# Performance work log

Measured on AMD Instinct MI355X. Metric: run time of the kernel, lower is better.

## Reference

```python
import jax, jax.numpy as jnp
import numpy as np
import math

DIM, NH, HD = 4096, 32, 128
B, S = 2, 2048
MAX_SEQ, INIT_SLICE = 4096, 2048  # init_slice = max_seq_len - max_prompt_size
NEG = -1e9


def setup_inputs() -> dict:
    key = jax.random.key(0)
    ks = jax.random.split(key, 6)
    x = jax.random.normal(ks[0], (B, S, DIM), dtype=jnp.float32)
    scale = 1.0 / math.sqrt(DIM)
    wq = jax.random.normal(ks[1], (DIM, DIM), dtype=jnp.float32) * scale
    wk = jax.random.normal(ks[2], (DIM, DIM), dtype=jnp.float32) * scale
    wv = jax.random.normal(ks[3], (DIM, DIM), dtype=jnp.float32) * scale
    wo = jax.random.normal(ks[4], (DIM, DIM), dtype=jnp.float32) * scale
    # RoPE frequencies, viewed as real pairs [S, HD//2, 2] = (cos, sin)
    inv_freq = 1.0 / (10000.0 ** (jnp.arange(0, HD, 2, dtype=jnp.float32) / HD))
    ang = jnp.arange(S, dtype=jnp.float32)[:, None] * inv_freq[None, :]  # [S, HD//2]
    freqs_cis_real = jnp.stack([jnp.cos(ang), jnp.sin(ang)], axis=-1)
    # causal additive mask [1,1,S,S]
    mask = jnp.where(jnp.triu(jnp.ones((S, S), dtype=bool), k=1), NEG, 0.0)[None, None].astype(jnp.float32)
    cache_k = jnp.zeros((B, MAX_SEQ, NH, HD), dtype=jnp.float32)
    cache_v = jnp.zeros((B, MAX_SEQ, NH, HD), dtype=jnp.float32)
    return {"x": x, "freqs_cis_real": freqs_cis_real, "mask": mask,
            "wq": wq, "wk": wk, "wv": wv, "wo": wo,
            "cache_k": cache_k, "cache_v": cache_v, "slice_size": 2048}


def _apply_rotary(xq, xk, freqs_cis_real):
    # xq, xk: [b, s, h, d]; pairs along last dim are (real, imag)
    b, s, h, d = xq.shape
    fr = freqs_cis_real[None, :, None, :, 0]  # [1, s, 1, d//2]
    fi = freqs_cis_real[None, :, None, :, 1]

    def rot(t):
        t = t.reshape(b, s, h, d // 2, 2)
        tr, ti = t[..., 0], t[..., 1]
        out = jnp.stack([tr * fr - ti * fi, tr * fi + ti * fr], axis=-1)
        return out.reshape(b, s, h, d)

    return rot(xq), rot(xk)


def reference(x, freqs_cis_real, mask, wq, wk, wv, wo, cache_k, cache_v, slice_size):
    bsz, seqlen, _ = x.shape
    xq = (x @ wq.T).reshape(bsz, seqlen, NH, HD)
    xk = (x @ wk.T).reshape(bsz, seqlen, NH, HD)
    xv = (x @ wv.T).reshape(bsz, seqlen, NH, HD)
    xq, xk = _apply_rotary(xq, xk, freqs_cis_real)
    # prompt-phase (seqlen > 1) cache update: cat(cache[:, :init_slice], new)
    cache_k_new = jnp.concatenate([cache_k[:bsz, :INIT_SLICE], xk], axis=1)
    cache_v_new = jnp.concatenate([cache_v[:bsz, :INIT_SLICE], xv], axis=1)
    keys = cache_k_new[:, -slice_size:]    # [b, k, h, d]
    values = cache_v_new[:, -slice_size:]
    scores = jnp.einsum('bqhd,bkhd->bhqk', xq, keys) / math.sqrt(HD)
    scores = scores + mask
    probs = jax.nn.softmax(scores.astype(jnp.float32), axis=-1).astype(xq.dtype)
    out = jnp.einsum('bhqk,bkhd->bqhd', probs, values).reshape(bsz, seqlen, -1)
    return out @ wo.T
```

## Files before the change

### kernel.cpp

```cpp
#include <hip/hip_runtime.h>
#include <hip/hip_bf16.h>
#include <stdint.h>

#define SEQ   2048
#define NHEAD 32
#define HDIM  128
#define DMODEL 4096
#define MTOT  4096
#define RSCALE 0.08838834764831845f

typedef __hip_bfloat16 bf16_t;
typedef __attribute__((ext_vector_type(8))) short short8v;
typedef __attribute__((ext_vector_type(4))) short short4v;
typedef __attribute__((ext_vector_type(4))) float f32x4;
typedef __attribute__((ext_vector_type(2))) float f32x2;

typedef __attribute__((address_space(3))) void lds_void;
typedef __attribute__((address_space(1))) void gbl_void;
#define TO_LDS(p) ((lds_void*)(uint32_t)(uintptr_t)(p))
#define TO_GBL(p) ((gbl_void*)(uintptr_t)(p))
#define ASYNC_CP16(g, l) __builtin_amdgcn_global_load_lds(TO_GBL(g), TO_LDS(l), 16, 0, 0)

__device__ __forceinline__ float bf2f(short u) {
  union { uint32_t i; float f; } x; x.i = ((uint32_t)(uint16_t)u) << 16; return x.f;
}

__global__ __launch_bounds__(256) void cast4_f32_to_bf16(const float* __restrict__ s0,
                                                         const float* __restrict__ s1,
                                                         const float* __restrict__ s2,
                                                         const float* __restrict__ s3,
                                                         bf16_t* __restrict__ out) {
  const int w = blockIdx.y;
  const float* in = (w == 0) ? s0 : ((w == 1) ? s1 : ((w == 2) ? s2 : s3));
  bf16_t* o = out + (size_t)w * 16777216u;
  size_t i = (size_t)blockIdx.x * 256 + threadIdx.x;
  const f32x4* p = (const f32x4*)in + i * 2;
  f32x4 a = p[0], b = p[1];
  __align__(16) bf16_t tmp[8];
#pragma unroll
  for (int j = 0; j < 4; ++j) tmp[j]     = __float2bfloat16(a[j]);
#pragma unroll
  for (int j = 0; j < 4; ++j) tmp[4 + j] = __float2bfloat16(b[j]);
  *(short8v*)(o + i * 8) = *(const short8v*)tmp;
}

#define VMW_(N) asm volatile("s_waitcnt vmcnt(" #N ")" ::: "memory")
#define VMW(N) VMW_(N)
#define SB0 __builtin_amdgcn_sched_barrier(0)

#define STAGE_A(mh_, X)                                                        \
  { const int tr_ = tid >> 3, c_ = tid & 7;                                    \
    _Pragma("unroll")                                                          \
    for (int i_ = 0; i_ < 2; ++i_) {                                           \
      const int row_ = (mh_) * 64 + i_ * 128 + tr_;                            \
      const int cg_ = c_ ^ (row_ & 7);                                         \
      ASYNC_CP16(gA0 + (size_t)row_ * 4096 + (size_t)(X) * 64 + cg_ * 8,       \
                 ldsc + (((X) & 1) << 16) + row_ * 128 + c_ * 16); } }

#define STAGE_B(nh_, X)                                                        \
  { const int tr_ = tid >> 3, c_ = tid & 7;                                    \
    _Pragma("unroll")                                                          \
    for (int i_ = 0; i_ < 2; ++i_) {                                           \
      const int row_ = i_ * 128 + (tr_ >> 5) * 64 + (nh_) * 32 + (tr_ & 31);   \
      const int cg_ = c_ ^ (row_ & 7);                                         \
      ASYNC_CP16(gB0 + (size_t)row_ * 4096 + (size_t)(X) * 64 + cg_ * 8,       \
                 ldsc + (((X) & 1) << 16) + 32768 + row_ * 128 + c_ * 16); } }

#define TILE4(T, DOSTG, VA, VB, VC)                                            \
  {                                                                            \
    const int sb = ((T) & 1) << 16;                                            \
    const int Xn = (T) + 1;                                                    \
    short8v a0[4][2], a1[4][2], b0[2][2], b1[2][2];                            \
                                                 \
    VMW(VA);                                                                   \
    __builtin_amdgcn_s_barrier();                                              \
    SB0;                                                                       \
    _Pragma("unroll") for (int m = 0; m < 4; ++m)                              \
      _Pragma("unroll") for (int kk = 0; kk < 2; ++kk)                         \
        a0[m][kk] = *(const short8v*)(ldsc + sb + aRow + m * 2048 + (kk ? cx1 : cx0)); \
    _Pragma("unroll") for (int n = 0; n < 2; ++n)                              \
      _Pragma("unroll") for (int kk = 0; kk < 2; ++kk)                         \
        b0[n][kk] = *(const short8v*)(ldsc + sb + bRow + n * 2048 + (kk ? cx1 : cx0)); \
    if (DOSTG) STAGE_A(0, Xn);                                                 \
    asm volatile("s_waitcnt lgkmcnt(0)" ::: "memory");                         \
    SB0;                                                                       \
    __builtin_amdgcn_s_setprio(1);                                             \
    _Pragma("unroll") for (int m = 0; m < 4; ++m)                              \
      _Pragma("unroll") for (int n = 0; n < 2; ++n)                            \
        _Pragma("unroll") for (int kk = 0; kk < 2; ++kk)                       \
          acc[m][n] = __builtin_amdgcn_mfma_f32_16x16x32_bf16(a0[m][kk], b0[n][kk], acc[m][n], 0, 0, 0); \
    __builtin_amdgcn_s_setprio(0);                                             \
                                                 \
    VMW(VB);                                                                   \
    __builtin_amdgcn_s_barrier();                                              \
    SB0;                                                                       \
    _Pragma("unroll") for (int n = 0; n < 2; ++n)                              \
      _Pragma("unroll") for (int kk = 0; kk < 2; ++kk)                         \
        b1[n][kk] = *(const short8v*)(ldsc + sb + bRow + 4096 + n * 2048 + (kk ? cx1 : cx0)); \
    if (DOSTG) STAGE_B(0, Xn);                                                 \
    asm volatile("s_waitcnt lgkmcnt(0)" ::: "memory");                         \
    SB0;                                                                       \
    __builtin_amdgcn_s_setprio(1);                                             \
    _Pragma("unroll") for (int m = 0; m < 4; ++m)                              \
      _Pragma("unroll") for (int n = 0; n < 2; ++n)                            \
        _Pragma("unroll") for (int kk = 0; kk < 2; ++kk)                       \
          acc[m][2 + n] = __builtin_amdgcn_mfma_f32_16x16x32_bf16(a0[m][kk], b1[n][kk], acc[m][2 + n], 0, 0, 0); \
    __builtin_amdgcn_s_setprio(0);                                             \
                                                 \
    VMW(VC);                                                                   \
    __builtin_amdgcn_s_barrier();                                              \
    SB0;                                                                       \
    _Pragma("unroll") for (int m = 0; m < 4; ++m)                              \
      _Pragma("unroll") for (int kk = 0; kk < 2; ++kk)                         \
        a1[m][kk] = *(const short8v*)(ldsc + sb + aRow + 8192 + m * 2048 + (kk ? cx1 : cx0)); \
    if (DOSTG) STAGE_B(1, Xn);                                                 \
    asm volatile("s_waitcnt lgkmcnt(0)" ::: "memory");                         \
    SB0;                                                                       \
    __builtin_amdgcn_s_setprio(1);                                             \
    _Pragma("unroll") for (int m = 0; m < 4; ++m)                              \
      _Pragma("unroll") for (int n = 0; n < 2; ++n)                            \
        _Pragma("unroll") for (int kk = 0; kk < 2; ++kk)                       \
          acc[4 + m][2 + n] = __builtin_amdgcn_mfma_f32_16x16x32_bf16(a1[m][kk], b1[n][kk], acc[4 + m][2 + n], 0, 0, 0); \
    __builtin_amdgcn_s_setprio(0);                                             \
                                     \
    if (DOSTG) STAGE_A(1, Xn);                                                 \
    __builtin_amdgcn_s_setprio(1);                                             \
    _Pragma("unroll") for (int m = 0; m < 4; ++m)                              \
      _Pragma("unroll") for (int n = 0; n < 2; ++n)                            \
        _Pragma("unroll") for (int kk = 0; kk < 2; ++kk)                       \
          acc[4 + m][n] = __builtin_amdgcn_mfma_f32_16x16x32_bf16(a1[m][kk], b0[n][kk], acc[4 + m][n], 0, 0, 0); \
    __builtin_amdgcn_s_setprio(0);                                             \
  }

template <int MODE>
__global__ __launch_bounds__(512, 2) void gemm_nt(const bf16_t* __restrict__ A,
                                                  const bf16_t* __restrict__ B0,
                                                  const bf16_t* __restrict__ B1,
                                                  const bf16_t* __restrict__ B2,
                                                  void* __restrict__ out0,
                                                  bf16_t* __restrict__ out1,
                                                  bf16_t* __restrict__ out2,
                                                  const float* __restrict__ freqs) {
  __shared__ __align__(16) char ldsbuf[131072];
  char* ldsc = ldsbuf;
  const int z = blockIdx.z;
  const bf16_t* __restrict__ Bm = (z == 0) ? B0 : (z == 1 ? B1 : B2);
  const int tid = threadIdx.x;
  const int wave = tid >> 6, lane = tid & 63;
  const int bid = blockIdx.x;
  const int xcd = bid & 7, idx = bid >> 3;
  const int bm = xcd * 2 + (idx >> 4);
  const int bn = idx & 15;
  const int wr = wave >> 2, wc = wave & 3;
  const int r = lane & 15, g = lane >> 4;

  f32x4 acc[8][4] = {};

  const bf16_t* gA0 = A  + (size_t)bm * 256 * 4096;
  const bf16_t* gB0 = Bm + (size_t)bn * 256 * 4096;

  const int swz = r & 7;
  const int cx0 = (g ^ swz) << 4;
  const int cx1 = ((4 + g) ^ swz) << 4;
  const int aRow = (wr * 128 + r) * 128;
  const int bRow = 32768 + (wc * 64 + r) * 128;

  STAGE_A(0, 0);
  STAGE_B(0, 0);
  STAGE_B(1, 0);
  STAGE_A(1, 0);

  for (int T = 0; T < 63; ++T) TILE4(T, 1, 4, 4, 4);
  TILE4(63, 0, 4, 2, 0);

  const int row0 = bm * 256 + wr * 128 + g * 4;
  const int col0 = bn * 256 + wc * 64;

  if (MODE == 0) {
    float* C = (float*)out0;
#pragma unroll
    for (int m = 0; m < 8; ++m)
#pragma unroll
      for (int n = 0; n < 4; ++n)
#pragma unroll
        for (int j = 0; j < 4; ++j)
          C[(size_t)(row0 + m * 16 + j) * 4096 + col0 + n * 16 + r] = acc[m][n][j];
  } else if (z == 2) {
    bf16_t* VT = out2;
#pragma unroll
    for (int m = 0; m < 8; ++m) {
      const int row = row0 + m * 16;
      const int b = row >> 11, s = row & 2047;
#pragma unroll
      for (int n = 0; n < 4; ++n) {
        const int col = col0 + n * 16 + r;
        const int h = col >> 7, d = col & 127;
        __align__(8) bf16_t tp[4];
#pragma unroll
        for (int j = 0; j < 4; ++j) tp[j] = __float2bfloat16(acc[m][n][j]);
        *(short4v*)&VT[((size_t)(b * 32 + h) * 128 + d) * 2048 + s] = *(const short4v*)tp;
      }
    }
  } else if (z == 0) {
    bf16_t* dst = (bf16_t*)out0;
#pragma unroll
    for (int m = 0; m < 8; ++m)
#pragma unroll
      for (int j = 0; j < 4; ++j) {
        const int row = row0 + m * 16 + j;
        const int b = row >> 11, s = row & 2047;
#pragma unroll
        for (int n = 0; n < 4; ++n) {
          const int col = col0 + n * 16 + r;
          const int h = col >> 7, d = col & 127;
          dst[((size_t)(b * 32 + h) * 2048 + s) * 128 + d] = __float2bfloat16(acc[m][n][j]);
        }
      }
  } else {
    bf16_t* dst = out1;
    const float sgn = (r & 1) ? 1.0f : -1.0f;
#pragma unroll
    for (int m = 0; m < 8; ++m)
#pragma unroll
      for (int j = 0; j < 4; ++j) {
        const int row = row0 + m * 16 + j;
        const int b = row >> 11, s = row & 2047;
#pragma unroll
        for (int n = 0; n < 4; ++n) {
          const int col = col0 + n * 16 + r;
          const int h = col >> 7, d = col & 127;
          const float self = acc[m][n][j];
          const float part = __shfl_xor(self, 1, 64);
          const float* fp = freqs + (size_t)s * 128 + (d >> 1) * 2;
          const float frv = fp[0];
          const float fiv = fp[1] * sgn;
          dst[((size_t)(b * 32 + h) * 2048 + s) * 128 + d] =
              __float2bfloat16(self * frv + part * fiv);
        }
      }
  }
}

__global__ __launch_bounds__(512) void attn_kernel(const bf16_t* __restrict__ qrot,
                                                   const bf16_t* __restrict__ krot,
                                                   const bf16_t* __restrict__ vt,
                                                   const float* __restrict__ freqs,
                                                   bf16_t* __restrict__ att,
                                                   const float* __restrict__ wo_src,
                                                   bf16_t* __restrict__ wo_dst) {
  __shared__ bf16_t Kls[2][64 * 128];
  __shared__ bf16_t Vls[2][128 * 64];
  __shared__ bf16_t Pls[8][16 * 64];

  if (blockIdx.x >= 1024) {
    const int cb = blockIdx.x - 1024;
    const int tid = threadIdx.x;
#pragma unroll
    for (int p = 0; p < 8; ++p) {
      size_t i = ((size_t)p * 512 + cb) * 512 + tid;
      const f32x4* pp = (const f32x4*)wo_src + i * 2;
      f32x4 a = pp[0], b = pp[1];
      __align__(16) bf16_t tmp[8];
#pragma unroll
      for (int j = 0; j < 4; ++j) tmp[j]     = __float2bfloat16(a[j]);
#pragma unroll
      for (int j = 0; j < 4; ++j) tmp[4 + j] = __float2bfloat16(b[j]);
      *(short8v*)(wo_dst + i * 8) = *(const short8v*)tmp;
    }
    return;
  }

  const int lid  = blockIdx.x;
  const int xcd  = lid & 7;
  const int kk_  = lid >> 3;
  const int bh   = xcd + 8 * ((kk_ >> 4) & 7);
  const int qidx = 15 - (kk_ & 15);
  const int warp = threadIdx.x >> 6;
  const int lane = threadIdx.x & 63;
  const int r = lane & 15, g = lane >> 4;

  const bf16_t* __restrict__ Q  = qrot + (size_t)bh * 2048 * 128;
  const bf16_t* __restrict__ Kp = krot + (size_t)bh * 2048 * 128;
  const bf16_t* __restrict__ Vt = vt   + (size_t)bh * 128 * 2048;
  char* __restrict__ Pb = (char*)&Pls[warp][0];

  const int qB = qidx * 128 + warp * 16;
  const int ntiles = 2 * qidx + 2;
  const int psw = (r & 7) << 4;

  short8v qf[4];
  {
    const int s = qB + r;
    const float* fbase = freqs + (size_t)s * 128;
#pragma unroll
    for (int kk = 0; kk < 4; ++kk) {
      short8v qraw = *(const short8v*)&Q[(size_t)s * 128 + kk * 32 + g * 8];
      __align__(16) bf16_t qt[8];
#pragma unroll
      for (int i = 0; i < 4; ++i) {
        const int p = kk * 16 + g * 4 + i;
        f32x2 cs = *(const f32x2*)(fbase + p * 2);
        const float a = bf2f(qraw[2 * i]), b = bf2f(qraw[2 * i + 1]);
        qt[2 * i]     = __float2bfloat16((a * cs[0] - b * cs[1]) * RSCALE);
        qt[2 * i + 1] = __float2bfloat16((a * cs[1] + b * cs[0]) * RSCALE);
      }
      qf[kk] = *(const short8v*)qt;
    }
  }

  float l = 0.f;
  f32x4 o[8];
#pragma unroll
  for (int n2 = 0; n2 < 8; ++n2) o[n2] = f32x4{0.f, 0.f, 0.f, 0.f};

  const int rA = lane >> 4, cA = lane & 15;
  const int rB = lane >> 3, cB = lane & 7;
  const int swz = (r & 7) << 4;

  auto STG = [&](int kb_, int buf) {
#pragma unroll
    for (int i = 0; i < 2; ++i) {
      const int krow = warp * 8 + i * 4 + rA;
      const int kcol = 8 * (cA ^ (krow & 7));
      ASYNC_CP16(Kp + (size_t)(kb_ + krow) * 128 + kcol,
                 (char*)&Kls[buf][0] + (size_t)(krow * 128 + cA * 8) * 2);
    }
#pragma unroll
    for (int i = 0; i < 2; ++i) {
      const int vrow = warp * 16 + i * 8 + rB;
      const int vcol = 8 * (cB ^ rB);
      ASYNC_CP16(Vt + (size_t)vrow * 2048 + kb_ + vcol,
                 (char*)&Vls[buf][0] + (size_t)(vrow * 64 + cB * 8) * 2);
    }
  };

  STG(0, 0);
  VMW(0);
  __builtin_amdgcn_s_barrier();
  int cur = 0;
  for (int t = 0; t < ntiles; ++t) {
    const int kb = t * 64;
    if (t + 1 < ntiles) STG(kb + 64, cur ^ 1);

    if (kb <= qB + 15) {
      const char* Kc = (const char*)&Kls[cur][0];
      const char* Vc = (const char*)&Vls[cur][0];
      f32x4 sacc[4];
#pragma unroll
      for (int n = 0; n < 4; ++n) sacc[n] = f32x4{0.f, 0.f, 0.f, 0.f};
#pragma unroll
      for (int n = 0; n < 4; ++n)
#pragma unroll
        for (int kk = 0; kk < 4; ++kk) {
          short8v kf = *(const short8v*)(Kc + (n * 16 + r) * 256 + ((kk * 64 + g * 16) ^ swz));
          sacc[n] = __builtin_amdgcn_mfma_f32_16x16x32_bf16(kf, qf[kk], sacc[n], 0, 0, 0);
        }

      float p[16];
#pragma unroll
      for (int n = 0; n < 4; ++n)
#pragma unroll
        for (int j = 0; j < 4; ++j)
          p[n * 4 + j] = __expf(sacc[n][j]);

      if (kb + 63 > qB) {
        const int qa = qB + r;
#pragma unroll
        for (int n = 0; n < 4; ++n)
#pragma unroll
          for (int j = 0; j < 4; ++j)
            if (kb + n * 16 + g * 4 + j > qa) p[n * 4 + j] = 0.f;
      }

      {
        float ts[8];
#pragma unroll
        for (int i = 0; i < 8; ++i) ts[i] = p[i] + p[i + 8];
#pragma unroll
        for (int i = 0; i < 4; ++i) ts[i] += ts[i + 4];
        float rs = (ts[0] + ts[1]) + (ts[2] + ts[3]);
        rs += __shfl_xor(rs, 16, 64);
        rs += __shfl_xor(rs, 32, 64);
        l += rs;
      }

#pragma unroll
      for (int n = 0; n < 4; ++n) {
        __align__(8) bf16_t tp[4];
#pragma unroll
        for (int j = 0; j < 4; ++j) tp[j] = __float2bfloat16(p[n * 4 + j]);
        *(short4v*)(Pb + r * 128 + ((n * 32 + g * 8) ^ psw)) = *(const short4v*)tp;
      }

#pragma unroll
      for (int kk2 = 0; kk2 < 2; ++kk2) {
        short8v pf = *(const short8v*)(Pb + r * 128 + ((kk2 * 64 + g * 16) ^ psw));
#pragma unroll
        for (int n2 = 0; n2 < 8; ++n2) {
          short8v vf = *(const short8v*)(Vc + (n2 * 16 + r) * 128 + ((kk2 * 64 + g * 16) ^ swz));
          o[n2] = __builtin_amdgcn_mfma_f32_16x16x32_bf16(pf, vf, o[n2], 0, 0, 0);
        }
      }
    }

    if (t + 1 < ntiles) {
      VMW(0);
      __builtin_amdgcn_s_barrier();
    }
    cur ^= 1;
  }

  float lq[4];
#pragma unroll
  for (int j = 0; j < 4; ++j) lq[j] = 1.0f / __shfl(l, g * 4 + j, 64);
  const int b = bh >> 5, h = bh & 31;
#pragma unroll
  for (int n2 = 0; n2 < 8; ++n2)
#pragma unroll
    for (int j = 0; j < 4; ++j)
      att[((size_t)(b * 2048 + qB + g * 4 + j)) * 4096 + h * 128 + n2 * 16 + r] =
          __float2bfloat16(o[n2][j] * lq[j]);
}

extern "C" void kernel_launch(void* const* d_in, const int* in_sizes, int n_in,
                              void* d_out, int out_size, void* d_ws, size_t ws_size,
                              hipStream_t stream) {
  (void)in_sizes; (void)n_in; (void)out_size; (void)ws_size;
  const float* x  = (const float*)d_in[0];
  const float* fr = (const float*)d_in[1];
  const float* wq = (const float*)d_in[3];
  const float* wk = (const float*)d_in[4];
  const float* wv = (const float*)d_in[5];
  const float* wo = (const float*)d_in[6];

  char* ws = (char*)d_ws;
  const size_t MB32 = 33554432;
  bf16_t* xb   = (bf16_t*)(ws + 0 * MB32);
  bf16_t* wqb  = (bf16_t*)(ws + 1 * MB32);
  bf16_t* wkb  = (bf16_t*)(ws + 2 * MB32);
  bf16_t* wvb  = (bf16_t*)(ws + 3 * MB32);
  bf16_t* qrot = (bf16_t*)(ws + 4 * MB32);
  bf16_t* krot = (bf16_t*)(ws + 5 * MB32);
  bf16_t* vtp  = (bf16_t*)(ws + 6 * MB32);

  cast4_f32_to_bf16<<<dim3(8192, 4), 256, 0, stream>>>(x, wq, wk, wv, xb);

  gemm_nt<1><<<dim3(256, 1, 3), 512, 0, stream>>>(xb, wqb, wkb, wvb,
                                                  (void*)qrot, krot, vtp, fr);

  bf16_t* wob  = wqb;
  bf16_t* attb = xb;

  attn_kernel<<<1536, 512, 0, stream>>>(qrot, krot, vtp, fr, attb, wo, wob);

  gemm_nt<0><<<dim3(256, 1, 1), 512, 0, stream>>>(attb, wob, wob, wob,
                                                  d_out, nullptr, nullptr, nullptr);
}
```

Before: 629.2 us.

## Load GEMM A operand directly from global into registers, stage only B in LDS

The projection GEMM kernel no longer stages the A tile through LDS. Each wave now loads its A fragments straight from global memory into registers, double-buffered across k-steps, while only the B tile is staged asynchronously into a halved LDS buffer. The wave layout also changes from 2x4 to 4x2 with 64x128 per-wave tiles, and the per-tile barriers drop from three to one. This cuts LDS traffic, LDS footprint and synchronisation, at the cost of uncoalesced global loads for A, more register pressure, and redundant A reads by the two waves that share each row block.

```diff
diff --git a/kernel.cpp b/kernel.cpp
--- a/kernel.cpp
+++ b/kernel.cpp
@@ -24,6 +24,10 @@
 __device__ __forceinline__ float bf2f(short u) {
   union { uint32_t i; float f; } x; x.i = ((uint32_t)(uint16_t)u) << 16; return x.f;
 }
+
+#define VMW_(N) asm volatile("s_waitcnt vmcnt(" #N ")" ::: "memory")
+#define VMW(N) VMW_(N)
+#define SB0 __builtin_amdgcn_sched_barrier(0)
 
 __global__ __launch_bounds__(256) void cast4_f32_to_bf16(const float* __restrict__ s0,
                                                          const float* __restrict__ s1,
@@ -44,92 +48,44 @@
   *(short8v*)(o + i * 8) = *(const short8v*)tmp;
 }
 
-#define VMW_(N) asm volatile("s_waitcnt vmcnt(" #N ")" ::: "memory")
-#define VMW(N) VMW_(N)
-#define SB0 __builtin_amdgcn_sched_barrier(0)
-
-#define STAGE_A(mh_, X)                                                        \
+#define STAGE_BT(slot_, X)                                                     \
   { const int tr_ = tid >> 3, c_ = tid & 7;                                    \
     _Pragma("unroll")                                                          \
-    for (int i_ = 0; i_ < 2; ++i_) {                                           \
-      const int row_ = (mh_) * 64 + i_ * 128 + tr_;                            \
-      const int cg_ = c_ ^ (row_ & 7);                                         \
-      ASYNC_CP16(gA0 + (size_t)row_ * 4096 + (size_t)(X) * 64 + cg_ * 8,       \
-                 ldsc + (((X) & 1) << 16) + row_ * 128 + c_ * 16); } }
-
-#define STAGE_B(nh_, X)                                                        \
-  { const int tr_ = tid >> 3, c_ = tid & 7;                                    \
-    _Pragma("unroll")                                                          \
-    for (int i_ = 0; i_ < 2; ++i_) {                                           \
-      const int row_ = i_ * 128 + (tr_ >> 5) * 64 + (nh_) * 32 + (tr_ & 31);   \
+    for (int i_ = 0; i_ < 4; ++i_) {                                           \
+      const int row_ = i_ * 64 + tr_;                                          \
       const int cg_ = c_ ^ (row_ & 7);                                         \
       ASYNC_CP16(gB0 + (size_t)row_ * 4096 + (size_t)(X) * 64 + cg_ * 8,       \
-                 ldsc + (((X) & 1) << 16) + 32768 + row_ * 128 + c_ * 16); } }
-
-#define TILE4(T, DOSTG, VA, VB, VC)                                            \
+                 ldsc + (slot_) * 32768 + row_ * 128 + c_ * 16); } }
+
+#define LDA(AR, X)                                                             \
+  _Pragma("unroll") for (int m_ = 0; m_ < 4; ++m_)                             \
+    _Pragma("unroll") for (int kk_ = 0; kk_ < 2; ++kk_)                        \
+      AR[m_][kk_] = *(const short8v*)(gA0 + (size_t)m_ * 65536 +               \
+                                      (size_t)(X) * 64 + kk_ * 32 + g * 8);
+
+#define GTILE(TT, AC, AN, DOSTG)                                               \
   {                                                                            \
-    const int sb = ((T) & 1) << 16;                                            \
-    const int Xn = (T) + 1;                                                    \
-    short8v a0[4][2], a1[4][2], b0[2][2], b1[2][2];                            \
-                                                 \
-    VMW(VA);                                                                   \
-    __builtin_amdgcn_s_barrier();                                              \
-    SB0;                                                                       \
-    _Pragma("unroll") for (int m = 0; m < 4; ++m)                              \
-      _Pragma("unroll") for (int kk = 0; kk < 2; ++kk)                         \
-        a0[m][kk] = *(const short8v*)(ldsc + sb + aRow + m * 2048 + (kk ? cx1 : cx0)); \
-    _Pragma("unroll") for (int n = 0; n < 2; ++n)                              \
-      _Pragma("unroll") for (int kk = 0; kk < 2; ++kk)                         \
-        b0[n][kk] = *(const short8v*)(ldsc + sb + bRow + n * 2048 + (kk ? cx1 : cx0)); \
-    if (DOSTG) STAGE_A(0, Xn);                                                 \
-    asm volatile("s_waitcnt lgkmcnt(0)" ::: "memory");                         \
-    SB0;                                                                       \
+    const int slot_c = (TT) & 1;                                               \
+    if (DOSTG) {                                                               \
+      STAGE_BT(slot_c ^ 1, (TT) + 1);                                          \
+      LDA(AN, (TT) + 1);                                                       \
+    }                                                                          \
     __builtin_amdgcn_s_setprio(1);                                             \
-    _Pragma("unroll") for (int m = 0; m < 4; ++m)                              \
-      _Pragma("unroll") for (int n = 0; n < 2; ++n)                            \
-        _Pragma("unroll") for (int kk = 0; kk < 2; ++kk)                       \
-          acc[m][n] = __builtin_amdgcn_mfma_f32_16x16x32_bf16(a0[m][kk], b0[n][kk], acc[m][n], 0, 0, 0); \
+    _Pragma("unroll") for (int n = 0; n < 8; ++n) {                            \
+      const char* bp = ldsc + slot_c * 32768 + bRow + n * 2048;                \
+      short8v b0 = *(const short8v*)(bp + cx0);                                \
+      short8v b1 = *(const short8v*)(bp + cx1);                                \
+      _Pragma("unroll") for (int m = 0; m < 4; ++m) {                          \
+        acc[m][n] = __builtin_amdgcn_mfma_f32_16x16x32_bf16(AC[m][0], b0, acc[m][n], 0, 0, 0); \
+        acc[m][n] = __builtin_amdgcn_mfma_f32_16x16x32_bf16(AC[m][1], b1, acc[m][n], 0, 0, 0); \
+      }                                                                        \
+    }                                                                          \
     __builtin_amdgcn_s_setprio(0);                                             \
-                                                 \
-    VMW(VB);                                                                   \
-    __builtin_amdgcn_s_barrier();                                              \
-    SB0;                                                                       \
-    _Pragma("unroll") for (int n = 0; n < 2; ++n)                              \
-      _Pragma("unroll") for (int kk = 0; kk < 2; ++kk)                         \
-        b1[n][kk] = *(const short8v*)(ldsc + sb + bRow + 4096 + n * 2048 + (kk ? cx1 : cx0)); \
-    if (DOSTG) STAGE_B(0, Xn);                                                 \
-    asm volatile("s_waitcnt lgkmcnt(0)" ::: "memory");                         \
-    SB0;                                                                       \
-    __builtin_amdgcn_s_setprio(1);                                             \
-    _Pragma("unroll") for (int m = 0; m < 4; ++m)                              \
-      _Pragma("unroll") for (int n = 0; n < 2; ++n)                            \
-        _Pragma("unroll") for (int kk = 0; kk < 2; ++kk)                       \
-          acc[m][2 + n] = __builtin_amdgcn_mfma_f32_16x16x32_bf16(a0[m][kk], b1[n][kk], acc[m][2 + n], 0, 0, 0); \
-    __builtin_amdgcn_s_setprio(0);                                             \
-                                                 \
-    VMW(VC);                                                                   \
-    __builtin_amdgcn_s_barrier();                                              \
-    SB0;                                                                       \
-    _Pragma("unroll") for (int m = 0; m < 4; ++m)                              \
-      _Pragma("unroll") for (int kk = 0; kk < 2; ++kk)                         \
-        a1[m][kk] = *(const short8v*)(ldsc + sb + aRow + 8192 + m * 2048 + (kk ? cx1 : cx0)); \
-    if (DOSTG) STAGE_B(1, Xn);                                                 \
-    asm volatile("s_waitcnt lgkmcnt(0)" ::: "memory");                         \
-    SB0;                                                                       \
-    __builtin_amdgcn_s_setprio(1);                                             \
-    _Pragma("unroll") for (int m = 0; m < 4; ++m)                              \
-      _Pragma("unroll") for (int n = 0; n < 2; ++n)                            \
-        _Pragma("unroll") for (int kk = 0; kk < 2; ++kk)                       \
-          acc[4 + m][2 + n] = __builtin_amdgcn_mfma_f32_16x16x32_bf16(a1[m][kk], b1[n][kk], acc[4 + m][2 + n], 0, 0, 0); \
-    __builtin_amdgcn_s_setprio(0);                                             \
-                                     \
-    if (DOSTG) STAGE_A(1, Xn);                                                 \
-    __builtin_amdgcn_s_setprio(1);                                             \
-    _Pragma("unroll") for (int m = 0; m < 4; ++m)                              \
-      _Pragma("unroll") for (int n = 0; n < 2; ++n)                            \
-        _Pragma("unroll") for (int kk = 0; kk < 2; ++kk)                       \
-          acc[4 + m][n] = __builtin_amdgcn_mfma_f32_16x16x32_bf16(a1[m][kk], b0[n][kk], acc[4 + m][n], 0, 0, 0); \
-    __builtin_amdgcn_s_setprio(0);                                             \
+    if (DOSTG) {                                                               \
+      VMW(8);                                                                  \
+      __builtin_amdgcn_s_barrier();                                            \
+      SB0;                                                                     \
+    }                                                                          \
   }
 
 template <int MODE>
@@ -141,7 +97,7 @@
                                                   bf16_t* __restrict__ out1,
                                                   bf16_t* __restrict__ out2,
                                                   const float* __restrict__ freqs) {
-  __shared__ __align__(16) char ldsbuf[131072];
+  __shared__ __align__(16) char ldsbuf[65536];
   char* ldsc = ldsbuf;
   const int z = blockIdx.z;
   const bf16_t* __restrict__ Bm = (z == 0) ? B0 : (z == 1 ? B1 : B2);
@@ -151,48 +107,54 @@
   const int xcd = bid & 7, idx = bid >> 3;
   const int bm = xcd * 2 + (idx >> 4);
   const int bn = idx & 15;
-  const int wr = wave >> 2, wc = wave & 3;
+  const int wr = wave >> 1, wc = wave & 1;
   const int r = lane & 15, g = lane >> 4;
 
-  f32x4 acc[8][4] = {};
-
-  const bf16_t* gA0 = A  + (size_t)bm * 256 * 4096;
+  f32x4 acc[4][8] = {};
+
+  const bf16_t* gA0 = A + ((size_t)(bm * 256 + wr * 64 + r)) * 4096;
   const bf16_t* gB0 = Bm + (size_t)bn * 256 * 4096;
 
   const int swz = r & 7;
   const int cx0 = (g ^ swz) << 4;
   const int cx1 = ((4 + g) ^ swz) << 4;
-  const int aRow = (wr * 128 + r) * 128;
-  const int bRow = 32768 + (wc * 64 + r) * 128;
-
-  STAGE_A(0, 0);
-  STAGE_B(0, 0);
-  STAGE_B(1, 0);
-  STAGE_A(1, 0);
-
-  for (int T = 0; T < 63; ++T) TILE4(T, 1, 4, 4, 4);
-  TILE4(63, 0, 4, 2, 0);
-
-  const int row0 = bm * 256 + wr * 128 + g * 4;
-  const int col0 = bn * 256 + wc * 64;
+  const int bRow = (wc * 128 + r) * 128;
+
+  short8v aA[4][2], aB[4][2];
+
+  STAGE_BT(0, 0);
+  LDA(aA, 0);
+  VMW(8);
+  __builtin_amdgcn_s_barrier();
+  SB0;
+
+  for (int T = 0; T < 62; T += 2) {
+    GTILE(T, aA, aB, 1);
+    GTILE(T + 1, aB, aA, 1);
+  }
+  GTILE(62, aA, aB, 1);
+  GTILE(63, aB, aA, 0);
+
+  const int row0 = bm * 256 + wr * 64 + g * 4;
+  const int col0 = bn * 256 + wc * 128;
 
   if (MODE == 0) {
     float* C = (float*)out0;
 #pragma unroll
-    for (int m = 0; m < 8; ++m)
-#pragma unroll
-      for (int n = 0; n < 4; ++n)
+    for (int m = 0; m < 4; ++m)
+#pragma unroll
+      for (int n = 0; n < 8; ++n)
 #pragma unroll
         for (int j = 0; j < 4; ++j)
           C[(size_t)(row0 + m * 16 + j) * 4096 + col0 + n * 16 + r] = acc[m][n][j];
   } else if (z == 2) {
     bf16_t* VT = out2;
 #pragma unroll
-    for (int m = 0; m < 8; ++m) {
+    for (int m = 0; m < 4; ++m) {
       const int row = row0 + m * 16;
       const int b = row >> 11, s = row & 2047;
 #pragma unroll
-      for (int n = 0; n < 4; ++n) {
+      for (int n = 0; n < 8; ++n) {
         const int col = col0 + n * 16 + r;
         const int h = col >> 7, d = col & 127;
         __align__(8) bf16_t tp[4];
@@ -204,13 +166,13 @@
   } else if (z == 0) {
     bf16_t* dst = (bf16_t*)out0;
 #pragma unroll
-    for (int m = 0; m < 8; ++m)
+    for (int m = 0; m < 4; ++m)
 #pragma unroll
       for (int j = 0; j < 4; ++j) {
         const int row = row0 + m * 16 + j;
         const int b = row >> 11, s = row & 2047;
 #pragma unroll
-        for (int n = 0; n < 4; ++n) {
+        for (int n = 0; n < 8; ++n) {
           const int col = col0 + n * 16 + r;
           const int h = col >> 7, d = col & 127;
           dst[((size_t)(b * 32 + h) * 2048 + s) * 128 + d] = __float2bfloat16(acc[m][n][j]);
@@ -220,13 +182,13 @@
     bf16_t* dst = out1;
     const float sgn = (r & 1) ? 1.0f : -1.0f;
 #pragma unroll
-    for (int m = 0; m < 8; ++m)
+    for (int m = 0; m < 4; ++m)
 #pragma unroll
       for (int j = 0; j < 4; ++j) {
         const int row = row0 + m * 16 + j;
         const int b = row >> 11, s = row & 2047;
 #pragma unroll
-        for (int n = 0; n < 4; ++n) {
+        for (int n = 0; n < 8; ++n) {
           const int col = col0 + n * 16 + r;
           const int h = col >> 7, d = col & 127;
           const float self = acc[m][n][j];
```

New measurement: 866.8 us. 37.8% more time.

## Restructure GEMM main loop into deeper prefetch pipeline with split-phase barriers

Applied to the files above, without the earlier changes.

Rewrites the bf16 NT GEMM inner loop so global-to-LDS async copies for tile T+2 are issued while tile T is computed, with tile T+1's B half staged early. Each of the four 64x... quadrant MFMA phases is bracketed by barriers and LDS reads are overlapped with outstanding loads via partial lgkmcnt waits. The intent is to hide global memory latency better and keep MFMA units busier, at the cost of more barriers per k-tile and tighter vmcnt bookkeeping that could serialize if miscounted.

```diff
diff --git a/kernel.cpp b/kernel.cpp
--- a/kernel.cpp
+++ b/kernel.cpp
@@ -24,6 +24,12 @@
 __device__ __forceinline__ float bf2f(short u) {
   union { uint32_t i; float f; } x; x.i = ((uint32_t)(uint16_t)u) << 16; return x.f;
 }
+
+#define VMW_(N) asm volatile("s_waitcnt vmcnt(" #N ")" ::: "memory")
+#define VMW(N) VMW_(N)
+#define SB0 __builtin_amdgcn_sched_barrier(0)
+#define LGKM0 asm volatile("s_waitcnt lgkmcnt(0)" ::: "memory")
+#define LGKM8 asm volatile("s_waitcnt lgkmcnt(8)" ::: "memory")
 
 __global__ __launch_bounds__(256) void cast4_f32_to_bf16(const float* __restrict__ s0,
                                                          const float* __restrict__ s1,
@@ -44,10 +50,6 @@
   *(short8v*)(o + i * 8) = *(const short8v*)tmp;
 }
 
-#define VMW_(N) asm volatile("s_waitcnt vmcnt(" #N ")" ::: "memory")
-#define VMW(N) VMW_(N)
-#define SB0 __builtin_amdgcn_sched_barrier(0)
-
 #define STAGE_A(mh_, X)                                                        \
   { const int tr_ = tid >> 3, c_ = tid & 7;                                    \
     _Pragma("unroll")                                                          \
@@ -66,70 +68,56 @@
       ASYNC_CP16(gB0 + (size_t)row_ * 4096 + (size_t)(X) * 64 + cg_ * 8,       \
                  ldsc + (((X) & 1) << 16) + 32768 + row_ * 128 + c_ * 16); } }
 
-#define TILE4(T, DOSTG, VA, VB, VC)                                            \
+#define RD_A(AR, SL, MH)                                                       \
+  _Pragma("unroll") for (int m_ = 0; m_ < 4; ++m_) {                           \
+    AR[m_][0] = *(const short8v*)(ldsc + (SL) + aRow + (MH) * 8192 + m_ * 2048 + cx0); \
+    AR[m_][1] = *(const short8v*)(ldsc + (SL) + aRow + (MH) * 8192 + m_ * 2048 + cx1); }
+
+#define RD_B(BR, SL, NH)                                                       \
+  _Pragma("unroll") for (int n_ = 0; n_ < 2; ++n_) {                           \
+    BR[n_][0] = *(const short8v*)(ldsc + (SL) + bRow + (NH) * 4096 + n_ * 2048 + cx0); \
+    BR[n_][1] = *(const short8v*)(ldsc + (SL) + bRow + (NH) * 4096 + n_ * 2048 + cx1); }
+
+#define MFMA16(AR, BR, MH, NH)                                                 \
+  __builtin_amdgcn_s_setprio(1);                                               \
+  _Pragma("unroll") for (int m_ = 0; m_ < 4; ++m_)                             \
+    _Pragma("unroll") for (int n_ = 0; n_ < 2; ++n_) {                         \
+      acc[(MH)*4+m_][(NH)*2+n_] = __builtin_amdgcn_mfma_f32_16x16x32_bf16(     \
+          AR[m_][0], BR[n_][0], acc[(MH)*4+m_][(NH)*2+n_], 0, 0, 0);           \
+      acc[(MH)*4+m_][(NH)*2+n_] = __builtin_amdgcn_mfma_f32_16x16x32_bf16(     \
+          AR[m_][1], BR[n_][1], acc[(MH)*4+m_][(NH)*2+n_], 0, 0, 0); }         \
+  __builtin_amdgcn_s_setprio(0);
+
+#define BAR __builtin_amdgcn_s_barrier()
+
+#define KTILE(T, SB1_, SA0_, SB0_, SA1_, VMC)                                  \
   {                                                                            \
-    const int sb = ((T) & 1) << 16;                                            \
-    const int Xn = (T) + 1;                                                    \
-    short8v a0[4][2], a1[4][2], b0[2][2], b1[2][2];                            \
-                                                 \
-    VMW(VA);                                                                   \
-    __builtin_amdgcn_s_barrier();                                              \
-    SB0;                                                                       \
-    _Pragma("unroll") for (int m = 0; m < 4; ++m)                              \
-      _Pragma("unroll") for (int kk = 0; kk < 2; ++kk)                         \
-        a0[m][kk] = *(const short8v*)(ldsc + sb + aRow + m * 2048 + (kk ? cx1 : cx0)); \
-    _Pragma("unroll") for (int n = 0; n < 2; ++n)                              \
-      _Pragma("unroll") for (int kk = 0; kk < 2; ++kk)                         \
-        b0[n][kk] = *(const short8v*)(ldsc + sb + bRow + n * 2048 + (kk ? cx1 : cx0)); \
-    if (DOSTG) STAGE_A(0, Xn);                                                 \
-    asm volatile("s_waitcnt lgkmcnt(0)" ::: "memory");                         \
-    SB0;                                                                       \
-    __builtin_amdgcn_s_setprio(1);                                             \
-    _Pragma("unroll") for (int m = 0; m < 4; ++m)                              \
-      _Pragma("unroll") for (int n = 0; n < 2; ++n)                            \
-        _Pragma("unroll") for (int kk = 0; kk < 2; ++kk)                       \
-          acc[m][n] = __builtin_amdgcn_mfma_f32_16x16x32_bf16(a0[m][kk], b0[n][kk], acc[m][n], 0, 0, 0); \
-    __builtin_amdgcn_s_setprio(0);                                             \
-                                                 \
-    VMW(VB);                                                                   \
-    __builtin_amdgcn_s_barrier();                                              \
-    SB0;                                                                       \
-    _Pragma("unroll") for (int n = 0; n < 2; ++n)                              \
-      _Pragma("unroll") for (int kk = 0; kk < 2; ++kk)                         \
-        b1[n][kk] = *(const short8v*)(ldsc + sb + bRow + 4096 + n * 2048 + (kk ? cx1 : cx0)); \
-    if (DOSTG) STAGE_B(0, Xn);                                                 \
-    asm volatile("s_waitcnt lgkmcnt(0)" ::: "memory");                         \
-    SB0;                                                                       \
-    __builtin_amdgcn_s_setprio(1);                                             \
-    _Pragma("unroll") for (int m = 0; m < 4; ++m)                              \
-      _Pragma("unroll") for (int n = 0; n < 2; ++n)                            \
-        _Pragma("unroll") for (int kk = 0; kk < 2; ++kk)                       \
-          acc[m][2 + n] = __builtin_amdgcn_mfma_f32_16x16x32_bf16(a0[m][kk], b1[n][kk], acc[m][2 + n], 0, 0, 0); \
-    __builtin_amdgcn_s_setprio(0);                                             \
-                                                 \
-    VMW(VC);                                                                   \
-    __builtin_amdgcn_s_barrier();                                              \
-    SB0;                                                                       \
-    _Pragma("unroll") for (int m = 0; m < 4; ++m)                              \
-      _Pragma("unroll") for (int kk = 0; kk < 2; ++kk)                         \
-        a1[m][kk] = *(const short8v*)(ldsc + sb + aRow + 8192 + m * 2048 + (kk ? cx1 : cx0)); \
-    if (DOSTG) STAGE_B(1, Xn);                                                 \
-    asm volatile("s_waitcnt lgkmcnt(0)" ::: "memory");                         \
-    SB0;                                                                       \
-    __builtin_amdgcn_s_setprio(1);                                             \
-    _Pragma("unroll") for (int m = 0; m < 4; ++m)                              \
-      _Pragma("unroll") for (int n = 0; n < 2; ++n)                            \
-        _Pragma("unroll") for (int kk = 0; kk < 2; ++kk)                       \
-          acc[4 + m][2 + n] = __builtin_amdgcn_mfma_f32_16x16x32_bf16(a1[m][kk], b1[n][kk], acc[4 + m][2 + n], 0, 0, 0); \
-    __builtin_amdgcn_s_setprio(0);                                             \
-                                     \
-    if (DOSTG) STAGE_A(1, Xn);                                                 \
-    __builtin_amdgcn_s_setprio(1);                                             \
-    _Pragma("unroll") for (int m = 0; m < 4; ++m)                              \
-      _Pragma("unroll") for (int n = 0; n < 2; ++n)                            \
-        _Pragma("unroll") for (int kk = 0; kk < 2; ++kk)                       \
-          acc[4 + m][n] = __builtin_amdgcn_mfma_f32_16x16x32_bf16(a1[m][kk], b0[n][kk], acc[4 + m][n], 0, 0, 0); \
-    __builtin_amdgcn_s_setprio(0);                                             \
+    const int sl = ((T) & 1) << 16;                                            \
+                                                               \
+    RD_A(a0, sl, 0); RD_B(b0, sl, 0);                                          \
+    if (SB1_) STAGE_B(1, (T) + 1);                                             \
+    LGKM8;                                                                     \
+    BAR; LGKM0; SB0;                                                           \
+    MFMA16(a0, b0, 0, 0);                                                      \
+    BAR;                                                                       \
+                                                               \
+    RD_A(a1, sl, 1);                                                           \
+    if (SA0_) STAGE_A(0, (T) + 2);                                             \
+    BAR; LGKM0; SB0;                                                           \
+    MFMA16(a1, b0, 1, 0);                                                      \
+    BAR;                                                                       \
+                                                               \
+    RD_B(b1, sl, 1);                                                           \
+    if (SB0_) STAGE_B(0, (T) + 2);                                             \
+    BAR; LGKM0; SB0;                                                           \
+    MFMA16(a1, b1, 1, 1);                                                      \
+    BAR;                                                                       \
+                    \
+    if (SA1_) STAGE_A(1, (T) + 2);                                             \
+    VMC;                                                                       \
+    BAR;                                                                       \
+    MFMA16(a0, b1, 0, 1);                                                      \
+    BAR;                                                                       \
   }
 
 template <int MODE>
@@ -165,13 +153,26 @@
   const int aRow = (wr * 128 + r) * 128;
   const int bRow = 32768 + (wc * 64 + r) * 128;
 
+  short8v a0[4][2], a1[4][2], b0[2][2], b1[2][2];
+
   STAGE_A(0, 0);
   STAGE_B(0, 0);
+  STAGE_A(1, 0);
   STAGE_B(1, 0);
-  STAGE_A(1, 0);
-
-  for (int T = 0; T < 63; ++T) TILE4(T, 1, 4, 4, 4);
-  TILE4(63, 0, 4, 2, 0);
+  VMW(4);
+  STAGE_A(0, 1);
+  STAGE_B(0, 1);
+  STAGE_A(1, 1);
+  VMW(6);
+  BAR;
+
+  for (int it = 0; it < 31; ++it) {
+    const int T0 = 2 * it;
+    KTILE(T0,     1, 1, 1, 1, VMW(6));
+    KTILE(T0 + 1, 1, 1, 1, 1, VMW(6));
+  }
+  KTILE(62, 1, 0, 0, 0, VMW(0));
+  KTILE(63, 0, 0, 0, 0, (void)0);
 
   const int row0 = bm * 256 + wr * 128 + g * 4;
   const int col0 = bn * 256 + wc * 64;
```

After: 639.4 us. No clear change (+1.6%).
